# Optimization experiments

Measured on AMD Instinct MI355X. Metric: run time of the kernel, lower is better.

## Reference

```python
import jax, jax.numpy as jnp
import numpy as np
from functools import partial

K = 0.5  # prune rate: keep top-k fraction of |popup_scores|


def get_subnet(scores, j):
    # Faithful to GetSubnet.forward: sort flattened scores ascending,
    # zero out the j smallest, set the rest to 1.
    flat = scores.ravel()
    idx = jnp.argsort(flat)
    mask = jnp.zeros_like(flat).at[idx[j:]].set(1.0)
    return mask.reshape(scores.shape)


def subnet_linear(x, w, s, b, k):
    j = int((1.0 - k) * w.size)  # static: shapes known at trace time
    adj = get_subnet(jnp.abs(s), j)
    return x @ (w * adj).T + b


def setup_inputs() -> dict:
    key = jax.random.key(0)
    ks = jax.random.split(key, 10)
    size_list = [2048, 4096, 4096, 1000]
    batch = 4096
    inp = {"x": jax.random.normal(ks[0], (batch, size_list[0]), dtype=jnp.float32)}
    for i in range(3):
        fan_out, fan_in = size_list[i + 1], size_list[i]
        bound = 1.0 / np.sqrt(fan_in)
        inp[f"w{i+1}"] = jax.random.uniform(ks[1 + 3 * i], (fan_out, fan_in), minval=-bound, maxval=bound, dtype=jnp.float32)
        inp[f"s{i+1}"] = jax.random.uniform(ks[2 + 3 * i], (fan_out, fan_in), minval=-bound, maxval=bound, dtype=jnp.float32)
        inp[f"b{i+1}"] = jax.random.uniform(ks[3 + 3 * i], (fan_out,), minval=-bound, maxval=bound, dtype=jnp.float32)
    return inp


def reference(x, w1, s1, b1, w2, s2, b2, w3, s3, b3):
    h = jax.nn.relu(subnet_linear(x, w1, s1, b1, K))
    h = jax.nn.relu(subnet_linear(h, w2, s2, b2, K))
    return subnet_linear(h, w3, s3, b3, K)
```

## Files before the change

kernel.cpp:

```cpp
#include <hip/hip_runtime.h>

typedef unsigned int u32;
typedef unsigned short u16;
typedef short s16x8 __attribute__((ext_vector_type(8)));
typedef __bf16 bf16x8 __attribute__((ext_vector_type(8)));
typedef float f32x4 __attribute__((ext_vector_type(4)));

#define KEYMASK 0x7fffffffu
#define NB1 1024
#define NB2 4096
#define CANDCAP 65536
#define TIECAP 2048

__device__ __forceinline__ u16 f2bf(float f) {
  u32 u = __builtin_bit_cast(u32, f);
  return (u16)((u + 0x7fffu + ((u >> 16) & 1u)) >> 16);
}

struct ABFrag {
  s16x8 v;
  __device__ operator s16x8() const { return v; }
  __device__ operator bf16x8() const { return __builtin_bit_cast(bf16x8, v); }
};

__device__ __forceinline__ f32x4 mfma_bf16(s16x8 a, s16x8 b, f32x4 c) {
  return __builtin_amdgcn_mfma_f32_16x16x32_bf16(ABFrag{a}, ABFrag{b}, c, 0, 0, 0);
}

__device__ __forceinline__ void async16(void* lds, const void* g) {
  __builtin_amdgcn_global_load_lds(
      (__attribute__((address_space(1))) void*)(const_cast<void*>(g)),
      (__attribute__((address_space(3))) void*)lds, 16, 0, 0);
}

__global__ void f32_to_bf16_k(const float4* __restrict__ in, ushort4* __restrict__ out, int n4) {
  int stride = gridDim.x * blockDim.x;
  for (int i = blockIdx.x * blockDim.x + threadIdx.x; i < n4; i += stride) {
    float4 v = in[i];
    ushort4 o;
    o.x = f2bf(v.x); o.y = f2bf(v.y); o.z = f2bf(v.z); o.w = f2bf(v.w);
    out[i] = o;
  }
}


__global__ void hist1_k(const uint4* __restrict__ sa, int na,
                        const uint4* __restrict__ sb, int nb,
                        const uint4* __restrict__ sc, int nc,
                        u32* __restrict__ gh) {
  __shared__ u32 h[3 * NB1 * 4];
  for (int i = threadIdx.x; i < 3 * NB1 * 4; i += blockDim.x) h[i] = 0;
  __syncthreads();
  const int rep = threadIdx.x & 3;
  const uint4* sp[3] = {sa, sb, sc};
  int nn[3] = {na, nb, nc};
  int stride = gridDim.x * blockDim.x;
  for (int l = 0; l < 3; ++l) {
    const uint4* s = sp[l];
    int n4 = nn[l];
    u32* hl = &h[l * NB1 * 4 + rep];
    for (int i = blockIdx.x * blockDim.x + threadIdx.x; i < n4; i += stride) {
      uint4 v = s[i];
      atomicAdd(&hl[((v.x & KEYMASK) >> 21) * 4], 1u);
      atomicAdd(&hl[((v.y & KEYMASK) >> 21) * 4], 1u);
      atomicAdd(&hl[((v.z & KEYMASK) >> 21) * 4], 1u);
      atomicAdd(&hl[((v.w & KEYMASK) >> 21) * 4], 1u);
    }
  }
  __syncthreads();
  for (int i = threadIdx.x; i < 3 * NB1; i += blockDim.x) {
    u32 c = h[i * 4] + h[i * 4 + 1] + h[i * 4 + 2] + h[i * 4 + 3];
    if (c) atomicAdd(&gh[i], c);
  }
}

__global__ void hist2_k(const uint4* __restrict__ sa, int na,
                        const uint4* __restrict__ sb, int nb,
                        const uint4* __restrict__ sc, int nc,
                        u32* __restrict__ gh, const u32* __restrict__ meta) {
  __shared__ u32 h[3 * NB2];
  for (int i = threadIdx.x; i < 3 * NB2; i += blockDim.x) h[i] = 0;
  __syncthreads();
  const uint4* sp[3] = {sa, sb, sc};
  int nn[3] = {na, nb, nc};
  int stride = gridDim.x * blockDim.x;
  for (int l = 0; l < 3; ++l) {
    const uint4* s = sp[l];
    int n4 = nn[l];
    u32 selA = meta[l * 8 + 0];
    u32* hl = &h[l * NB2];
    for (int i = blockIdx.x * blockDim.x + threadIdx.x; i < n4; i += stride) {
      uint4 v = s[i];
      u32 k;
      k = v.x & KEYMASK; if ((k >> 21) == selA) atomicAdd(&hl[(k >> 9) & 0xfffu], 1u);
      k = v.y & KEYMASK; if ((k >> 21) == selA) atomicAdd(&hl[(k >> 9) & 0xfffu], 1u);
      k = v.z & KEYMASK; if ((k >> 21) == selA) atomicAdd(&hl[(k >> 9) & 0xfffu], 1u);
      k = v.w & KEYMASK; if ((k >> 21) == selA) atomicAdd(&hl[(k >> 9) & 0xfffu], 1u);
    }
  }
  __syncthreads();
  for (int i = threadIdx.x; i < 3 * NB2; i += blockDim.x) {
    u32 c = h[i];
    if (c) atomicAdd(&gh[i], c);
  }
}

template <int STAGE>
__global__ void select_k(const u32* __restrict__ hist, u32* __restrict__ meta,
                         u32 r0, u32 r1, u32 r2) {
  const int l = blockIdx.x;
  const int nbins = (STAGE == 1) ? NB1 : NB2;
  const u32* hl = hist + l * nbins;
  __shared__ u32 part[256];
  int tid = threadIdx.x;
  int chunk = nbins >> 8;
  u32 sm = 0;
  for (int i = tid * chunk; i < (tid + 1) * chunk; ++i) sm += hl[i];
  part[tid] = sm;
  __syncthreads();
  if (tid == 0) {
    u32 r = (STAGE == 1) ? (l == 0 ? r0 : (l == 1 ? r1 : r2)) : meta[l * 8 + 1];
    u32 c = 0; int t = 0;
    for (; t < 256; ++t) { if (c + part[t] > r) break; c += part[t]; }
    u32 rr = r - c;
    int bin = t * chunk;
    for (;;) { u32 hv = hl[bin]; if (rr < hv) break; rr -= hv; ++bin; }
    if (STAGE == 1) { meta[l * 8 + 0] = (u32)bin; meta[l * 8 + 1] = rr; }
    else           { meta[l * 8 + 2] = (u32)bin; meta[l * 8 + 3] = rr; }
  }
}

__global__ void build_k(const float4* __restrict__ w, const uint4* __restrict__ s,
                        ushort4* __restrict__ wb, int n4,
                        u32* __restrict__ meta, uint2* __restrict__ cand) {
  u32 t22 = (meta[0] << 12) | meta[2];
  int stride = gridDim.x * blockDim.x;
  for (int i = blockIdx.x * blockDim.x + threadIdx.x; i < n4; i += stride) {
    uint4 sv = s[i];
    float4 wv = w[i];
    u32 k0 = sv.x & KEYMASK, k1 = sv.y & KEYMASK, k2 = sv.z & KEYMASK, k3 = sv.w & KEYMASK;
    ushort4 o;
    o.x = ((k0 >> 9) > t22) ? f2bf(wv.x) : (u16)0;
    o.y = ((k1 >> 9) > t22) ? f2bf(wv.y) : (u16)0;
    o.z = ((k2 >> 9) > t22) ? f2bf(wv.z) : (u16)0;
    o.w = ((k3 >> 9) > t22) ? f2bf(wv.w) : (u16)0;
    wb[i] = o;
    u32 base = (u32)i * 4u;
    if ((k0 >> 9) == t22) { u32 p = atomicAdd(&meta[4], 1u); if (p < CANDCAP) cand[p] = make_uint2(k0, base); }
    if ((k1 >> 9) == t22) { u32 p = atomicAdd(&meta[4], 1u); if (p < CANDCAP) cand[p] = make_uint2(k1, base + 1u); }
    if ((k2 >> 9) == t22) { u32 p = atomicAdd(&meta[4], 1u); if (p < CANDCAP) cand[p] = make_uint2(k2, base + 2u); }
    if ((k3 >> 9) == t22) { u32 p = atomicAdd(&meta[4], 1u); if (p < CANDCAP) cand[p] = make_uint2(k3, base + 3u); }
  }
}

__global__ void finalize_k(u16* __restrict__ wb, const float* __restrict__ w,
                           const u32* __restrict__ meta, const uint2* __restrict__ cand) {
  __shared__ u32 h[512];
  __shared__ u32 tie[TIECAP];
  __shared__ u32 tcnt, t9s, qs;
  int tid = threadIdx.x;
  for (int i = tid; i < 512; i += blockDim.x) h[i] = 0;
  if (tid == 0) tcnt = 0;
  __syncthreads();
  u32 m = meta[4]; if (m > CANDCAP) m = CANDCAP;
  for (u32 i = tid; i < m; i += blockDim.x) atomicAdd(&h[cand[i].x & 0x1ffu], 1u);
  __syncthreads();
  if (tid == 0) {
    u32 r = meta[3];
    u32 c = 0; int bin = 0;
    for (;;) { u32 hv = h[bin]; if (c + hv > r) break; c += hv; ++bin; }
    t9s = (u32)bin; qs = r - c;
  }
  __syncthreads();
  u32 t9 = t9s, q = qs;
  for (u32 i = tid; i < m; i += blockDim.x) {
    uint2 cd = cand[i];
    u32 k9 = cd.x & 0x1ffu;
    if (k9 > t9) wb[cd.y] = f2bf(w[cd.y]);
    else if (k9 == t9) { u32 p = atomicAdd(&tcnt, 1u); if (p < TIECAP) tie[p] = cd.y; }
  }
  __syncthreads();
  u32 tc = tcnt; if (tc > TIECAP) tc = TIECAP;
  for (u32 i = tid; i < tc; i += blockDim.x) {
    u32 my = tie[i];
    u32 rk = 0;
    for (u32 j = 0; j < tc; ++j) rk += (tie[j] < my) ? 1u : 0u;
    if (rk >= q) wb[my] = f2bf(w[my]);
  }
}

__global__ __launch_bounds__(512, 2) void gemm256(
    const u16* __restrict__ A, const u16* __restrict__ B,
    const float* __restrict__ bias, u16* __restrict__ C,
    int N, int K) {
  __shared__ __align__(16) u16 As[2][256 * 64];
  __shared__ __align__(16) u16 Bs[2][256 * 64];
  const int tid = threadIdx.x;
  const int lane = tid & 63;
  const int wv = tid >> 6;
  const int wm = wv >> 2;
  const int wn = wv & 3;
  const int fr = lane & 15;
  const int fkg = lane >> 4;
  const long brow = (long)blockIdx.y * 256;
  const long bcol = (long)blockIdx.x * 256;

  const int srow = tid >> 3;
  const int sgran = (tid & 7) ^ (srow & 7);
  const u16* pA[4];
  const u16* pB[4];
#pragma unroll
  for (int j = 0; j < 4; ++j) {
    pA[j] = A + (size_t)(brow + j * 64 + srow) * (size_t)K + sgran * 8;
    pB[j] = B + (size_t)(bcol + j * 64 + srow) * (size_t)K + sgran * 8;
  }
  char* lA[2]; char* lB[2];
  lA[0] = (char*)&As[0][0] + wv * 1024;
  lA[1] = (char*)&As[1][0] + wv * 1024;
  lB[0] = (char*)&Bs[0][0] + wv * 1024;
  lB[1] = (char*)&Bs[1][0] + wv * 1024;

  const int NT = K >> 6;

#pragma unroll
  for (int j = 0; j < 4; ++j) { async16(lA[0] + j * 8192, pA[j]); async16(lB[0] + j * 8192, pB[j]); }
#pragma unroll
  for (int j = 0; j < 4; ++j) { async16(lA[1] + j * 8192, pA[j] + 64); async16(lB[1] + j * 8192, pB[j] + 64); }

  f32x4 acc[8][4] = {};
  const int kswz = (fr & 7) << 4;

  for (int t = 0; t < NT; ++t) {
    if (t < NT - 1) { asm volatile("s_waitcnt vmcnt(8)" ::: "memory"); }
    else           { asm volatile("s_waitcnt vmcnt(0)" ::: "memory"); }
    __builtin_amdgcn_sched_barrier(0);
    __builtin_amdgcn_s_barrier();
    __builtin_amdgcn_sched_barrier(0);

    const char* Ab = (const char*)&As[t & 1][0];
    const char* Bb = (const char*)&Bs[t & 1][0];
#pragma unroll
    for (int ks = 0; ks < 2; ++ks) {
      const int ko = (ks * 64 + fkg * 16) ^ kswz;
      s16x8 a[8], b[4];
#pragma unroll
      for (int mf = 0; mf < 8; ++mf)
        a[mf] = *(const s16x8*)(Ab + (wm * 128 + mf * 16 + fr) * 128 + ko);
#pragma unroll
      for (int nf = 0; nf < 4; ++nf)
        b[nf] = *(const s16x8*)(Bb + (wn * 64 + nf * 16 + fr) * 128 + ko);
      __builtin_amdgcn_s_setprio(1);
#pragma unroll
      for (int mf = 0; mf < 8; ++mf)
#pragma unroll
        for (int nf = 0; nf < 4; ++nf)
          acc[mf][nf] = mfma_bf16(a[mf], b[nf], acc[mf][nf]);
      __builtin_amdgcn_s_setprio(0);
    }

    __builtin_amdgcn_sched_barrier(0);
    __builtin_amdgcn_s_barrier();
    __builtin_amdgcn_sched_barrier(0);

    if (t + 2 < NT) {
      const int kt = (t + 2) << 6;
      char* dA = lA[t & 1]; char* dB = lB[t & 1];
#pragma unroll
      for (int j = 0; j < 4; ++j) { async16(dA + j * 8192, pA[j] + kt); async16(dB + j * 8192, pB[j] + kt); }
    }
  }

#pragma unroll
  for (int nf = 0; nf < 4; ++nf) {
    const long col = bcol + wn * 64 + nf * 16 + fr;
    const float bv = bias[col];
#pragma unroll
    for (int mf = 0; mf < 8; ++mf) {
      const long row0 = brow + wm * 128 + mf * 16 + fkg * 4;
#pragma unroll
      for (int i = 0; i < 4; ++i) {
        float v = fmaxf(acc[mf][nf][i] + bv, 0.0f);
        C[(row0 + i) * (long)N + col] = f2bf(v);
      }
    }
  }
}

template <int RELU, int CBF16>
__global__ __launch_bounds__(256) void gemm_bt(
    const u16* __restrict__ A, const u16* __restrict__ B,
    const float* __restrict__ bias, void* __restrict__ Cv,
    int Ntrue, int K) {
  __shared__ __align__(16) u16 As[128 * 32];
  __shared__ __align__(16) u16 Bs[128 * 32];
  const int tid = threadIdx.x;
  const int lane = tid & 63;
  const int wv = tid >> 6;
  const long brow = (long)blockIdx.y * 128;
  const long bcol = (long)blockIdx.x * 128;
  const int wm = (wv >> 1) * 64;
  const int wn = (wv & 1) * 64;

  const u16* gA0 = A + (brow + (tid >> 2)) * (long)K + (tid & 3) * 8;
  const u16* gA1 = gA0 + (size_t)64 * K;
  const u16* gB0 = B + (bcol + (tid >> 2)) * (long)K + (tid & 3) * 8;
  const u16* gB1 = gB0 + (size_t)64 * K;
  char* lA0 = (char*)As + wv * 1024;
  char* lA1 = (char*)As + 4096 + wv * 1024;
  char* lB0 = (char*)Bs + wv * 1024;
  char* lB1 = (char*)Bs + 4096 + wv * 1024;

  f32x4 acc[4][4] = {};
  const int fr = lane & 15;
  const int fk = (lane >> 4) * 8;

  for (int kt = 0; kt < K; kt += 32) {
    async16(lA0, gA0 + kt);
    async16(lA1, gA1 + kt);
    async16(lB0, gB0 + kt);
    async16(lB1, gB1 + kt);
    __syncthreads();
    s16x8 a[4], b[4];
#pragma unroll
    for (int m = 0; m < 4; ++m) a[m] = *(const s16x8*)&As[(wm + m * 16 + fr) * 32 + fk];
#pragma unroll
    for (int n = 0; n < 4; ++n) b[n] = *(const s16x8*)&Bs[(wn + n * 16 + fr) * 32 + fk];
#pragma unroll
    for (int m = 0; m < 4; ++m)
#pragma unroll
      for (int n = 0; n < 4; ++n)
        acc[m][n] = mfma_bf16(a[m], b[n], acc[m][n]);
    __syncthreads();
  }

  const long col0 = bcol + wn + fr;
  const long row0 = brow + wm + ((lane >> 4) << 2);
#pragma unroll
  for (int n = 0; n < 4; ++n) {
    long col = col0 + n * 16;
    if (!CBF16 && col >= Ntrue) continue;
    float bv = bias[col];
#pragma unroll
    for (int m = 0; m < 4; ++m) {
#pragma unroll
      for (int i = 0; i < 4; ++i) {
        float v = acc[m][n][i] + bv;
        if (RELU) v = fmaxf(v, 0.0f);
        long off = (row0 + m * 16 + i) * (long)Ntrue + col;
        if (CBF16) ((u16*)Cv)[off] = f2bf(v);
        else ((float*)Cv)[off] = v;
      }
    }
  }
}

extern "C" void kernel_launch(void* const* d_in, const int* in_sizes, int n_in,
                              void* d_out, int out_size, void* d_ws, size_t ws_size,
                              hipStream_t stream) {
  const float* x  = (const float*)d_in[0];
  const float* w1 = (const float*)d_in[1];
  const float* s1 = (const float*)d_in[2];
  const float* b1 = (const float*)d_in[3];
  const float* w2 = (const float*)d_in[4];
  const float* s2 = (const float*)d_in[5];
  const float* b2 = (const float*)d_in[6];
  const float* w3 = (const float*)d_in[7];
  const float* s3 = (const float*)d_in[8];
  const float* b3 = (const float*)d_in[9];
  float* out = (float*)d_out;

  const int n1 = 4096 * 2048, n2 = 4096 * 4096, n3 = 1000 * 4096;

  char* ws = (char*)d_ws;
  u32*   meta = (u32*)ws;
  u32*   gh1  = (u32*)(ws + 0x1000);
  u32*   gh2  = (u32*)(ws + 0x4000);
  uint2* cand = (uint2*)(ws + 0x10000);
  u16* Wb = (u16*)(ws + (2l  << 20));
  u16* H1 = (u16*)(ws + (34l << 20));
  u16* H2 = (u16*)(ws + (66l << 20));
  u16* Xb = (u16*)(ws + (66l << 20));

  f32_to_bf16_k<<<1024, 256, 0, stream>>>((const float4*)x, (ushort4*)Xb, n1 / 4);

  hipMemsetAsync(ws, 0, 0x10000, stream);
  hist1_k<<<256, 1024, 0, stream>>>((const uint4*)s1, n1 / 4, (const uint4*)s2, n2 / 4,
                                    (const uint4*)s3, n3 / 4, gh1);
  select_k<1><<<3, 256, 0, stream>>>(gh1, meta, (u32)(n1 / 2), (u32)(n2 / 2), (u32)(n3 / 2));
  hist2_k<<<256, 1024, 0, stream>>>((const uint4*)s1, n1 / 4, (const uint4*)s2, n2 / 4,
                                    (const uint4*)s3, n3 / 4, gh2, meta);
  select_k<2><<<3, 256, 0, stream>>>(gh2, meta, 0, 0, 0);

  build_k<<<512, 256, 0, stream>>>((const float4*)w1, (const uint4*)s1, (ushort4*)Wb,
                                   n1 / 4, meta + 0, cand + 0);
  finalize_k<<<1, 1024, 0, stream>>>(Wb, w1, meta + 0, cand + 0);
  gemm256<<<dim3(16, 16), 512, 0, stream>>>(Xb, Wb, b1, H1, 4096, 2048);

  build_k<<<512, 256, 0, stream>>>((const float4*)w2, (const uint4*)s2, (ushort4*)Wb,
                                   n2 / 4, meta + 8, cand + CANDCAP);
  finalize_k<<<1, 1024, 0, stream>>>(Wb, w2, meta + 8, cand + CANDCAP);
  gemm256<<<dim3(16, 16), 512, 0, stream>>>(H1, Wb, b2, H2, 4096, 4096);

  build_k<<<512, 256, 0, stream>>>((const float4*)w3, (const uint4*)s3, (ushort4*)Wb,
                                   n3 / 4, meta + 16, cand + 2 * CANDCAP);
  finalize_k<<<1, 1024, 0, stream>>>(Wb, w3, meta + 16, cand + 2 * CANDCAP);
  hipMemsetAsync((char*)Wb + (size_t)1000 * 4096 * 2, 0, (size_t)24 * 4096 * 2, stream);
  gemm_bt<0, 0><<<dim3(8, 32), 256, 0, stream>>>(H2, Wb, b3, out, 1000, 4096);
}
```

Measured before the change: 491.0 us.

## Split GEMM main loop into four barrier phases with staggered async loads

Restructures the 256x256 bf16 GEMM main loop so each k-tile runs as four phases, each loading a 64-row A quarter and issuing part of the next tiles' async global-to-LDS copies between MFMA bursts. B fragments are held in registers across phases, and the A row mapping changes so quarters are interleaved. The goal is to overlap global loads with compute more finely and keep register pressure lower. Dropping the 2-blocks-per-CU launch bound and adding extra barriers can change occupancy and add sync overhead. Out-of-range prefetches are redirected to k=0 rather than skipped, which wastes some bandwidth.

```diff
diff --git a/kernel.cpp b/kernel.cpp
--- a/kernel.cpp
+++ b/kernel.cpp
@@ -189,7 +189,7 @@
   }
 }
 
-__global__ __launch_bounds__(512, 2) void gemm256(
+__global__ __launch_bounds__(512) void gemm256(
     const u16* __restrict__ A, const u16* __restrict__ B,
     const float* __restrict__ bias, u16* __restrict__ C,
     int N, int K) {
@@ -205,70 +205,160 @@
   const long brow = (long)blockIdx.y * 256;
   const long bcol = (long)blockIdx.x * 256;
 
-  const int srow = tid >> 3;
-  const int sgran = (tid & 7) ^ (srow & 7);
-  const u16* pA[4];
-  const u16* pB[4];
-#pragma unroll
-  for (int j = 0; j < 4; ++j) {
-    pA[j] = A + (size_t)(brow + j * 64 + srow) * (size_t)K + sgran * 8;
-    pB[j] = B + (size_t)(bcol + j * 64 + srow) * (size_t)K + sgran * 8;
-  }
-  char* lA[2]; char* lB[2];
-  lA[0] = (char*)&As[0][0] + wv * 1024;
-  lA[1] = (char*)&As[1][0] + wv * 1024;
-  lB[0] = (char*)&Bs[0][0] + wv * 1024;
-  lB[1] = (char*)&Bs[1][0] + wv * 1024;
+  const int sr6 = tid >> 3;
+  const int sgr = ((tid & 7) ^ (sr6 & 7)) << 3;
+  const int ha = tid >> 8;
+  const int ra = sr6 & 31;
+  const u16* pAq[4];
+  const u16* pBc[4];
+#pragma unroll
+  for (int q = 0; q < 4; ++q)
+    pAq[q] = A + (size_t)(brow + ha * 128 + q * 32 + ra) * (size_t)K + sgr;
+#pragma unroll
+  for (int c = 0; c < 4; ++c)
+    pBc[c] = B + (size_t)(bcol + c * 64 + sr6) * (size_t)K + sgr;
+
+  f32x4 acc[8][4] = {};
+  s16x8 bfr[4][2];
+
+  const int swz0 = ((0 + fkg) ^ (fr & 7)) * 16;
+  const int swz1 = ((4 + fkg) ^ (fr & 7)) * 16;
+
+  const int aRowBase = wm * 32 + fr;
+  const int bRowBase = wn * 64 + fr;
+
+  {
+    char* a0 = (char*)&As[0][0] + wv * 1024;
+    char* b0 = (char*)&Bs[0][0] + wv * 1024;
+    async16(a0 + 0 * 8192, pAq[0]); async16(a0 + 1 * 8192, pAq[1]); async16(a0 + 2 * 8192, pAq[2]);
+    async16(b0 + 0 * 8192, pBc[0]); async16(b0 + 1 * 8192, pBc[1]);
+    async16(b0 + 2 * 8192, pBc[2]); async16(b0 + 3 * 8192, pBc[3]);
+    async16(a0 + 3 * 8192, pAq[3]);
+    char* a1 = (char*)&As[1][0] + wv * 1024;
+    char* b1 = (char*)&Bs[1][0] + wv * 1024;
+    async16(a1 + 0 * 8192, pAq[0] + 64); async16(a1 + 1 * 8192, pAq[1] + 64); async16(a1 + 2 * 8192, pAq[2] + 64);
+    async16(b1 + 0 * 8192, pBc[0] + 64); async16(b1 + 1 * 8192, pBc[1] + 64);
+    async16(b1 + 2 * 8192, pBc[2] + 64); async16(b1 + 3 * 8192, pBc[3] + 64);
+  }
 
   const int NT = K >> 6;
 
-#pragma unroll
-  for (int j = 0; j < 4; ++j) { async16(lA[0] + j * 8192, pA[j]); async16(lB[0] + j * 8192, pB[j]); }
-#pragma unroll
-  for (int j = 0; j < 4; ++j) { async16(lA[1] + j * 8192, pA[j] + 64); async16(lB[1] + j * 8192, pB[j] + 64); }
-
-  f32x4 acc[8][4] = {};
-  const int kswz = (fr & 7) << 4;
-
   for (int t = 0; t < NT; ++t) {
-    if (t < NT - 1) { asm volatile("s_waitcnt vmcnt(8)" ::: "memory"); }
-    else           { asm volatile("s_waitcnt vmcnt(0)" ::: "memory"); }
+    const int p = t & 1;
+    const char* Ab = (const char*)&As[p][0];
+    const char* Bb = (const char*)&Bs[p][0];
+    char* sA = (char*)&As[p][0] + wv * 1024;
+    char* sB = (char*)&Bs[p][0] + wv * 1024;
+    char* sAo = (char*)&As[p ^ 1][0] + wv * 1024;
+    const int k1 = (t + 1 < NT ? t + 1 : 0) << 6;
+    const int k2 = (t + 2 < NT ? t + 2 : 0) << 6;
+
+    asm volatile("s_waitcnt vmcnt(8)" ::: "memory");
     __builtin_amdgcn_sched_barrier(0);
     __builtin_amdgcn_s_barrier();
     __builtin_amdgcn_sched_barrier(0);
-
-    const char* Ab = (const char*)&As[t & 1][0];
-    const char* Bb = (const char*)&Bs[t & 1][0];
-#pragma unroll
-    for (int ks = 0; ks < 2; ++ks) {
-      const int ko = (ks * 64 + fkg * 16) ^ kswz;
-      s16x8 a[8], b[4];
-#pragma unroll
-      for (int mf = 0; mf < 8; ++mf)
-        a[mf] = *(const s16x8*)(Ab + (wm * 128 + mf * 16 + fr) * 128 + ko);
-#pragma unroll
-      for (int nf = 0; nf < 4; ++nf)
-        b[nf] = *(const s16x8*)(Bb + (wn * 64 + nf * 16 + fr) * 128 + ko);
+    {
+#pragma unroll
+      for (int nf = 0; nf < 4; ++nf) {
+        const char* rb = Bb + (bRowBase + nf * 16) * 128;
+        bfr[nf][0] = *(const s16x8*)(rb + swz0);
+        bfr[nf][1] = *(const s16x8*)(rb + swz1);
+      }
+      s16x8 a_[2][2];
+#pragma unroll
+      for (int j = 0; j < 2; ++j) {
+        const char* rb = Ab + (0 * 64 + aRowBase + j * 16) * 128;
+        a_[j][0] = *(const s16x8*)(rb + swz0);
+        a_[j][1] = *(const s16x8*)(rb + swz1);
+      }
+      async16(sAo + 3 * 8192, pAq[3] + k1);
       __builtin_amdgcn_s_setprio(1);
 #pragma unroll
-      for (int mf = 0; mf < 8; ++mf)
-#pragma unroll
-        for (int nf = 0; nf < 4; ++nf)
-          acc[mf][nf] = mfma_bf16(a[mf], b[nf], acc[mf][nf]);
+      for (int j = 0; j < 2; ++j)
+#pragma unroll
+        for (int kk = 0; kk < 2; ++kk)
+#pragma unroll
+          for (int nf = 0; nf < 4; ++nf)
+            acc[j][nf] = mfma_bf16(a_[j][kk], bfr[nf][kk], acc[j][nf]);
       __builtin_amdgcn_s_setprio(0);
     }
 
     __builtin_amdgcn_sched_barrier(0);
     __builtin_amdgcn_s_barrier();
     __builtin_amdgcn_sched_barrier(0);
-
-    if (t + 2 < NT) {
-      const int kt = (t + 2) << 6;
-      char* dA = lA[t & 1]; char* dB = lB[t & 1];
-#pragma unroll
-      for (int j = 0; j < 4; ++j) { async16(dA + j * 8192, pA[j] + kt); async16(dB + j * 8192, pB[j] + kt); }
-    }
-  }
+    {
+      s16x8 a_[2][2];
+#pragma unroll
+      for (int j = 0; j < 2; ++j) {
+        const char* rb = Ab + (1 * 64 + aRowBase + j * 16) * 128;
+        a_[j][0] = *(const s16x8*)(rb + swz0);
+        a_[j][1] = *(const s16x8*)(rb + swz1);
+      }
+      async16(sA + 0 * 8192, pAq[0] + k2);
+      async16(sB + 0 * 8192, pBc[0] + k2);
+      __builtin_amdgcn_s_setprio(1);
+#pragma unroll
+      for (int j = 0; j < 2; ++j)
+#pragma unroll
+        for (int kk = 0; kk < 2; ++kk)
+#pragma unroll
+          for (int nf = 0; nf < 4; ++nf)
+            acc[2 + j][nf] = mfma_bf16(a_[j][kk], bfr[nf][kk], acc[2 + j][nf]);
+      __builtin_amdgcn_s_setprio(0);
+    }
+
+    __builtin_amdgcn_sched_barrier(0);
+    __builtin_amdgcn_s_barrier();
+    __builtin_amdgcn_sched_barrier(0);
+    {
+      s16x8 a_[2][2];
+#pragma unroll
+      for (int j = 0; j < 2; ++j) {
+        const char* rb = Ab + (2 * 64 + aRowBase + j * 16) * 128;
+        a_[j][0] = *(const s16x8*)(rb + swz0);
+        a_[j][1] = *(const s16x8*)(rb + swz1);
+      }
+      async16(sA + 1 * 8192, pAq[1] + k2);
+      async16(sB + 1 * 8192, pBc[1] + k2);
+      __builtin_amdgcn_s_setprio(1);
+#pragma unroll
+      for (int j = 0; j < 2; ++j)
+#pragma unroll
+        for (int kk = 0; kk < 2; ++kk)
+#pragma unroll
+          for (int nf = 0; nf < 4; ++nf)
+            acc[4 + j][nf] = mfma_bf16(a_[j][kk], bfr[nf][kk], acc[4 + j][nf]);
+      __builtin_amdgcn_s_setprio(0);
+    }
+
+    asm volatile("s_waitcnt vmcnt(12)" ::: "memory");
+    __builtin_amdgcn_sched_barrier(0);
+    __builtin_amdgcn_s_barrier();
+    __builtin_amdgcn_sched_barrier(0);
+    {
+      s16x8 a_[2][2];
+#pragma unroll
+      for (int j = 0; j < 2; ++j) {
+        const char* rb = Ab + (3 * 64 + aRowBase + j * 16) * 128;
+        a_[j][0] = *(const s16x8*)(rb + swz0);
+        a_[j][1] = *(const s16x8*)(rb + swz1);
+      }
+      async16(sA + 2 * 8192, pAq[2] + k2);
+      async16(sB + 2 * 8192, pBc[2] + k2);
+      async16(sB + 3 * 8192, pBc[3] + k2);
+      __builtin_amdgcn_s_setprio(1);
+#pragma unroll
+      for (int j = 0; j < 2; ++j)
+#pragma unroll
+        for (int kk = 0; kk < 2; ++kk)
+#pragma unroll
+          for (int nf = 0; nf < 4; ++nf)
+            acc[6 + j][nf] = mfma_bf16(a_[j][kk], bfr[nf][kk], acc[6 + j][nf]);
+      __builtin_amdgcn_s_setprio(0);
+    }
+  }
+
+  asm volatile("s_waitcnt vmcnt(0)" ::: "memory");
 
 #pragma unroll
   for (int nf = 0; nf < 4; ++nf) {
```

Measured after the change: 455.8 us. -7.2%, faster.
